# Optimization experiments

Hardware: AMD Instinct MI355X
Metric: run time of the kernel (lower is better)

## Reference

```python
import jax, jax.numpy as jnp
import numpy as np


def setup_inputs() -> dict:
    key = jax.random.key(0)
    ks = jax.random.split(key, 6)
    T, B, E = 2048, 4, 768
    x = jax.random.normal(ks[0], (T, B, E), dtype=jnp.float32)
    key_padding_mask = jax.random.randint(ks[1], (T, B), 0, 2).astype(jnp.bool_)
    attn_bias = jax.random.normal(ks[2], (T, B), dtype=jnp.float32)  # (src_len, bsz)
    in_proj_weight = jax.random.normal(ks[3], (3 * E, E), dtype=jnp.float32) * 0.02
    in_proj_bias = jnp.zeros((3 * E,), dtype=jnp.float32)
    out_weight = jax.random.normal(ks[4], (E, E), dtype=jnp.float32) * 0.02
    out_bias = jnp.zeros((E,), dtype=jnp.float32)
    return {
        "x": x,
        "key_padding_mask": key_padding_mask,
        "attn_bias": attn_bias,
        "in_proj_weight": in_proj_weight,
        "in_proj_bias": in_proj_bias,
        "out_weight": out_weight,
        "out_bias": out_bias,
        "num_heads": 12,
    }


def reference(x, key_padding_mask, attn_bias, in_proj_weight, in_proj_bias,
              out_weight, out_bias, num_heads):
    T, B, E = x.shape
    H = num_heads
    Dh = E // H
    scaling = Dh ** (-0.5)

    # fused QKV projection (self-attention path: q=k=v=x)
    qkv = x @ in_proj_weight.T + in_proj_bias        # (T, B, 3E)
    q, k, v = jnp.split(qkv, 3, axis=-1)             # each (T, B, E)
    q = q * scaling

    # (T, B, E) -> (B, H, T, Dh)
    def to_heads(t):
        return t.reshape(T, B, H, Dh).transpose(1, 2, 0, 3)
    q, k, v = to_heads(q), to_heads(k), to_heads(v)

    # scores: (B, H, T_tgt, T_src)
    scores = jnp.einsum('bhtd,bhsd->bhts', q, k)
    scores = scores + attn_bias.T[:, None, None, :]              # bias over src
    neg_inf = jnp.asarray(-jnp.inf, dtype=scores.dtype)
    scores = jnp.where(key_padding_mask.T[:, None, None, :], neg_inf, scores)

    weights = jax.nn.softmax(scores, axis=-1)
    attn = jnp.einsum('bhts,bhsd->bhtd', weights, v)             # (B, H, T, Dh)
    attn = attn.transpose(2, 0, 1, 3).reshape(T, B, E)           # (T, B, E)
    out = attn @ out_weight.T + out_bias
    return out
```

## Files before the change

### kernel.cpp

```cpp
#include <hip/hip_runtime.h>
#include <math.h>

#define T_LEN 2048
#define BSZ   4
#define EMB   768
#define NH    12
#define DH    64
#define NTOK  (T_LEN * BSZ)
#define N_QKV (3 * EMB)
#define BH    (BSZ * NH)
#define CONVB 8448

typedef _Float16 f16;
typedef _Float16 f16x8 __attribute__((ext_vector_type(8)));
typedef _Float16 f16x4 __attribute__((ext_vector_type(4)));
typedef float    f32x4 __attribute__((ext_vector_type(4)));

#define MFMA32(a, b, c) __builtin_amdgcn_mfma_f32_16x16x32_f16(a, b, c, 0, 0, 0)
#define MFMA16(a, b, c) __builtin_amdgcn_mfma_f32_16x16x16f16(a, b, c, 0, 0, 0)

__device__ __forceinline__ void gload16(const void* g, void* l) {
    __builtin_amdgcn_global_load_lds(
        (const __attribute__((address_space(1))) void*)g,
        (__attribute__((address_space(3))) void*)l, 16, 0, 0);
}

__global__ __launch_bounds__(256) void conv_compact(
    const float* __restrict__ s0, const float* __restrict__ s1,
    const float* __restrict__ s2, f16* __restrict__ dst,
    const int* __restrict__ mask, const float* __restrict__ abias,
    int* __restrict__ cidx, float* __restrict__ cbias,
    int* __restrict__ imap, int* __restrict__ ccount)
{
    const int tid = threadIdx.x;
    if (blockIdx.x < CONVB) {
        const int n0 = NTOK * EMB, n1 = N_QKV * EMB, n2 = EMB * EMB;
        const int i = (blockIdx.x * 256 + tid) * 4;
        const int t01 = n0 + n1;
        const float* s;
        int off;
        if (i < n0)            { s = s0; off = i; }
        else if (i < t01)      { s = s1; off = i - n0; }
        else if (i < t01 + n2) { s = s2; off = i - t01; }
        else return;
        const float4 v = *(const float4*)(s + off);
        f16 hv[4] = {(f16)v.x, (f16)v.y, (f16)v.z, (f16)v.w};
        *(double*)(dst + i) = *(double*)hv;
        return;
    }

    const int b = blockIdx.x - CONVB;
    __shared__ int cnt[32], off_l[32], tot[2];
    const int wv = tid >> 6, lane = tid & 63;
    int* ip = cidx + b * T_LEN;
    float* bp = cbias + b * T_LEN;
    int* mp = imap + b * T_LEN;

    for (int i = 0; i < 8; ++i) {
        const int c = wv * 8 + i;
        const int s = c * 64 + lane;
        const int mv = mask[s * BSZ + b];
        const unsigned long long bal = __ballot(mv == 0);
        if (lane == 0) cnt[c] = __popcll(bal);
    }
    __syncthreads();
    if (tid == 0) {
        int acc = 0;
        for (int c = 0; c < 32; ++c) { off_l[c] = acc; acc += cnt[c]; }
        const int npad = (acc + 63) & ~63;
        tot[0] = acc; tot[1] = npad;
        ccount[b] = npad;
    }
    __syncthreads();
    for (int i = 0; i < 8; ++i) {
        const int c = wv * 8 + i;
        const int s = c * 64 + lane;
        const int mv = mask[s * BSZ + b];
        const float bv = abias[s * BSZ + b];
        const unsigned long long bal = __ballot(mv == 0);
        const int pos = __popcll(bal & ((1ull << lane) - 1ull));
        const int basec = off_l[c];
        if (mv == 0) { ip[basec + pos] = s; bp[basec + pos] = bv; mp[s] = basec + pos; }
        else mp[s] = -1;
    }
    const int baseT = tot[0], npad = tot[1];
    if (tid < npad - baseT) { ip[baseT + tid] = 0; bp[baseT + tid] = -1e30f; }
}

template <int MODE>
__global__ __launch_bounds__(256) void gemm_h(
    const f16* __restrict__ A, const f16* __restrict__ W,
    const float* __restrict__ bias, float* __restrict__ C,
    f16* __restrict__ qb, f16* __restrict__ kc, f16* __restrict__ vb,
    const int* __restrict__ imap, int M, int N, int K)
{
    __shared__ __align__(16) f16 As[128][32];
    __shared__ __align__(16) f16 Bs[128][32];

    const int tid = threadIdx.x;
    const int w = tid >> 6, l = tid & 63;
    const int wr = w >> 1, wc = w & 1;
    const int lg = l >> 4, lr = l & 15;

    const int bm = blockIdx.x * 128, bn = blockIdx.y * 128;

    int srow[2], sqc[2];
#pragma unroll
    for (int it = 0; it < 2; ++it) {
        const int c = w * 128 + it * 64 + l;
        srow[it] = c >> 2;
        sqc[it] = (c & 3) ^ ((srow[it] >> 1) & 3);
    }

    f32x4 acc[4][4];
#pragma unroll
    for (int i = 0; i < 4; ++i)
#pragma unroll
        for (int j = 0; j < 4; ++j) acc[i][j] = (f32x4)(0.f);

    const int cq = lg ^ ((lr >> 1) & 3);

    for (int kt = 0; kt < K; kt += 32) {
        __syncthreads();
#pragma unroll
        for (int it = 0; it < 2; ++it) {
            const int ldsb = (w * 128 + it * 64) * 16;
            gload16(A + (size_t)(bm + srow[it]) * K + kt + sqc[it] * 8,
                    (char*)&As[0][0] + ldsb);
            gload16(W + (size_t)(bn + srow[it]) * K + kt + sqc[it] * 8,
                    (char*)&Bs[0][0] + ldsb);
        }
        __syncthreads();

        f16x8 af[4], bf[4];
#pragma unroll
        for (int am = 0; am < 4; ++am)
            af[am] = *(const f16x8*)((const char*)&As[0][0] +
                     (wr * 64 + am * 16 + lr) * 64 + cq * 16);
#pragma unroll
        for (int bnf = 0; bnf < 4; ++bnf)
            bf[bnf] = *(const f16x8*)((const char*)&Bs[0][0] +
                      (wc * 64 + bnf * 16 + lr) * 64 + cq * 16);
#pragma unroll
        for (int am = 0; am < 4; ++am)
#pragma unroll
            for (int bnf = 0; bnf < 4; ++bnf)
                acc[am][bnf] = MFMA32(af[am], bf[bnf], acc[am][bnf]);
    }

    const int colb = bn + wc * 64;
    const int rowb = bm + wr * 64;
    float bv[4];
#pragma unroll
    for (int j = 0; j < 4; ++j) bv[j] = bias[colb + j * 16 + lr];

    if (MODE == 0) {
#pragma unroll
        for (int am = 0; am < 4; ++am)
#pragma unroll
            for (int bnf = 0; bnf < 4; ++bnf)
#pragma unroll
                for (int rg = 0; rg < 4; ++rg) {
                    const int row = rowb + am * 16 + lg * 4 + rg;
                    const int col = colb + bnf * 16 + lr;
                    C[(size_t)row * N + col] = acc[am][bnf][rg] + bv[bnf];
                }
    } else {
        const int sec = bn / EMB;
        const float scale = (sec == 0) ? 0.125f : 1.0f;
#pragma unroll
        for (int bnf = 0; bnf < 4; ++bnf) {
            const int col = colb + bnf * 16 + lr;
            const int e = col - sec * EMB;
            const int h = e >> 6, d = e & 63;
#pragma unroll
            for (int am = 0; am < 4; ++am)
#pragma unroll
                for (int rg = 0; rg < 4; ++rg) {
                    const int row = rowb + am * 16 + lg * 4 + rg;
                    const int t = row >> 2, bb = row & 3;
                    const f16 val = (f16)((acc[am][bnf][rg] + bv[bnf]) * scale);
                    if (sec == 0) {
                        qb[((size_t)((bb * NH + h) * T_LEN + t)) * DH + d] = val;
                    } else if (sec == 1) {
                        const int ipv = imap[bb * T_LEN + t];
                        if (ipv >= 0)
                            kc[((size_t)((bb * NH + h) * T_LEN + ipv)) * DH + d] = val;
                    } else {
                        vb[((size_t)((bb * NH + h) * T_LEN + t)) * DH + d] = val;
                    }
                }
        }
    }
}

__global__ __launch_bounds__(256) void gather_vT(
    const f16* __restrict__ vb, const int* __restrict__ cidx,
    const int* __restrict__ ccnt, f16* __restrict__ vct)
{
    __shared__ f16 Vl[64][72];
    const int bh = blockIdx.y, b = bh / NH;
    const int i0 = blockIdx.x * 64;
    if (i0 >= ccnt[b]) return;
    const int tid = threadIdx.x;
    const size_t base = (size_t)bh * T_LEN * DH;

#pragma unroll
    for (int half = 0; half < 2; ++half) {
        const int c = half * 256 + tid;
        const int row = c >> 3, cc = c & 7;
        const int src = cidx[b * T_LEN + i0 + row];
        *(int4*)&Vl[row][cc * 8] =
            *(const int4*)(vb + base + (size_t)src * DH + cc * 8);
    }
    __syncthreads();
    const int dr = tid >> 2, ic = tid & 3;
    f16 tmp[16];
#pragma unroll
    for (int jj = 0; jj < 16; ++jj) tmp[jj] = Vl[ic * 16 + jj][dr];
    f16* dst = vct + ((size_t)bh * DH + dr) * T_LEN + i0 + ic * 16;
    *(int4*)(dst)     = *(int4*)&tmp[0];
    *(int4*)(dst + 8) = *(int4*)&tmp[8];
}

__global__ __launch_bounds__(256) void attn_mfma(
    const f16* __restrict__ qh, const f16* __restrict__ kcb,
    const f16* __restrict__ vct, const float* __restrict__ cbias,
    const int* __restrict__ ccnt, f16* __restrict__ abh)
{
    __shared__ __align__(16) f16 Kt[2][64][64];
    __shared__ __align__(16) f16 Vt[2][64][64];
    __shared__ float bias_l[2][64];

    const int bh = blockIdx.y, b = bh / NH, h = bh % NH;
    const int tid = threadIdx.x, w = tid >> 6, l = tid & 63;
    const int lg = l >> 4, lr = l & 15;
    const size_t base = (size_t)bh * T_LEN * DH;
    const int q0 = blockIdx.x * 128 + w * 32;

    f16x8 qf[2][2];
#pragma unroll
    for (int mi = 0; mi < 2; ++mi)
#pragma unroll
        for (int ki = 0; ki < 2; ++ki)
            qf[mi][ki] = *(const f16x8*)(qh + base +
                (size_t)(q0 + mi * 16 + lr) * DH + ki * 32 + lg * 8);

    f32x4 o[4][2];
#pragma unroll
    for (int dt = 0; dt < 4; ++dt)
#pragma unroll
        for (int mi = 0; mi < 2; ++mi) o[dt][mi] = (f32x4)(0.f);
    float m_[2] = {-1e30f, -1e30f}, l_[2] = {0.f, 0.f};

    const int npad = ccnt[b];
    const float* biasp = cbias + b * T_LEN;
    const f16* kbase = kcb + base;
    const f16* vtbase = vct + (size_t)bh * DH * T_LEN;

    int srow[2], scc[2];
#pragma unroll
    for (int it = 0; it < 2; ++it) {
        const int c = w * 128 + it * 64 + l;
        srow[it] = c >> 3;
        scc[it] = (c & 7) ^ (srow[it] & 7);
    }

    auto stage = [&](int buf, int i0s) {
#pragma unroll
        for (int it = 0; it < 2; ++it) {
            const int ldsb = (w * 128 + it * 64) * 16;
            gload16(kbase + (size_t)(i0s + srow[it]) * DH + scc[it] * 8,
                    (char*)&Kt[buf][0][0] + ldsb);
            gload16(vtbase + (size_t)srow[it] * T_LEN + i0s + scc[it] * 8,
                    (char*)&Vt[buf][0][0] + ldsb);
        }
        if (tid < 64) bias_l[buf][tid] = biasp[i0s + tid];
    };

    stage(0, 0);
    __syncthreads();

    int cur = 0;
    for (int i0 = 0; i0 < npad; i0 += 64, cur ^= 1) {
        if (i0 + 64 < npad) stage(cur ^ 1, i0 + 64);

        f32x4 s[4][2];
#pragma unroll
        for (int ni = 0; ni < 4; ++ni)
#pragma unroll
            for (int mi = 0; mi < 2; ++mi) s[ni][mi] = (f32x4)(0.f);
#pragma unroll
        for (int ni = 0; ni < 4; ++ni) {
            const int row = ni * 16 + lr;
#pragma unroll
            for (int ki = 0; ki < 2; ++ki) {
                const int cq = (ki * 4 + lg) ^ (row & 7);
                const f16x8 kf = *(const f16x8*)((const char*)&Kt[cur][0][0] +
                                 row * 128 + cq * 16);
#pragma unroll
                for (int mi = 0; mi < 2; ++mi)
                    s[ni][mi] = MFMA32(kf, qf[mi][ki], s[ni][mi]);
            }
        }

        float bv[4][4];
#pragma unroll
        for (int ni = 0; ni < 4; ++ni) {
            const float4 b4 = *(const float4*)&bias_l[cur][ni * 16 + lg * 4];
            bv[ni][0] = b4.x; bv[ni][1] = b4.y; bv[ni][2] = b4.z; bv[ni][3] = b4.w;
        }

        f16x4 pk[2][4];
        float r_[2];
#pragma unroll
        for (int mi = 0; mi < 2; ++mi) {
            float sv[4][4];
            float mx = -1e30f;
#pragma unroll
            for (int ni = 0; ni < 4; ++ni)
#pragma unroll
                for (int rg = 0; rg < 4; ++rg) {
                    sv[ni][rg] = s[ni][mi][rg] + bv[ni][rg];
                    mx = fmaxf(mx, sv[ni][rg]);
                }
            mx = fmaxf(mx, __shfl_xor(mx, 16));
            mx = fmaxf(mx, __shfl_xor(mx, 32));
            const float newm = fmaxf(m_[mi], mx);
            r_[mi] = __expf(m_[mi] - newm);
            m_[mi] = newm;
            float ps = 0.f;
#pragma unroll
            for (int ni = 0; ni < 4; ++ni) {
                float p0 = __expf(sv[ni][0] - newm);
                float p1 = __expf(sv[ni][1] - newm);
                float p2 = __expf(sv[ni][2] - newm);
                float p3 = __expf(sv[ni][3] - newm);
                ps += (p0 + p1) + (p2 + p3);
                pk[mi][ni] = (f16x4){(f16)p0, (f16)p1, (f16)p2, (f16)p3};
            }
            ps += __shfl_xor(ps, 16);
            ps += __shfl_xor(ps, 32);
            l_[mi] = l_[mi] * r_[mi] + ps;
        }

#pragma unroll
        for (int dt = 0; dt < 4; ++dt)
#pragma unroll
            for (int mi = 0; mi < 2; ++mi)
#pragma unroll
                for (int rg = 0; rg < 4; ++rg) o[dt][mi][rg] *= r_[mi];

#pragma unroll
        for (int dt = 0; dt < 4; ++dt) {
            const int row = dt * 16 + lr;
#pragma unroll
            for (int ni = 0; ni < 4; ++ni) {
                const int swc = (ni * 2 + (lg >> 1)) ^ (row & 7);
                const f16x4 vf = *(const f16x4*)((const char*)&Vt[cur][0][0] +
                                 row * 128 + swc * 16 + (lg & 1) * 8);
#pragma unroll
                for (int mi = 0; mi < 2; ++mi)
                    o[dt][mi] = MFMA16(vf, pk[mi][ni], o[dt][mi]);
            }
        }
        __syncthreads();
    }

#pragma unroll
    for (int mi = 0; mi < 2; ++mi) {
        const float inv = 1.f / l_[mi];
        const int q = q0 + mi * 16 + lr;
#pragma unroll
        for (int dt = 0; dt < 4; ++dt) {
            const int d0 = dt * 16 + lg * 4;
            f16x4 ov = {(f16)(o[dt][mi][0] * inv), (f16)(o[dt][mi][1] * inv),
                        (f16)(o[dt][mi][2] * inv), (f16)(o[dt][mi][3] * inv)};
            *(f16x4*)(abh + (size_t)(q * BSZ + b) * EMB + h * DH + d0) = ov;
        }
    }
}

extern "C" void kernel_launch(void* const* d_in, const int* in_sizes, int n_in,
                              void* d_out, int out_size, void* d_ws, size_t ws_size,
                              hipStream_t stream)
{
    const float* x     = (const float*)d_in[0];
    const int*   mask  = (const int*)d_in[1];
    const float* abias = (const float*)d_in[2];
    const float* wqkv  = (const float*)d_in[3];
    const float* bqkv  = (const float*)d_in[4];
    const float* wout  = (const float*)d_in[5];
    const float* bout  = (const float*)d_in[6];
    float* out = (float*)d_out;

    const int n_x  = NTOK * EMB;
    const int n_wq = N_QKV * EMB;
    const int n_wo = EMB * EMB;
    const size_t per = (size_t)BH * T_LEN * DH;

    f16* xh    = (f16*)d_ws;
    f16* wqkvh = xh + n_x;
    f16* wouth = wqkvh + n_wq;
    f16* qhb   = wouth + n_wo;
    f16* kcb   = qhb + per;
    f16* vhb   = kcb + per;
    f16* abh   = vhb + per;
    f16* vct   = abh + per;
    float* cbias = (float*)(vct + per);
    int*   cidx  = (int*)(cbias + BSZ * T_LEN);
    int*   imap  = cidx + BSZ * T_LEN;
    int*   ccnt  = imap + BSZ * T_LEN;

    conv_compact<<<CONVB + BSZ, 256, 0, stream>>>(
        x, wqkv, wout, xh, mask, abias, cidx, cbias, imap, ccnt);

    gemm_h<1><<<dim3(NTOK / 128, N_QKV / 128), 256, 0, stream>>>(
        xh, wqkvh, bqkv, nullptr, qhb, kcb, vhb, imap, NTOK, N_QKV, EMB);

    gather_vT<<<dim3(T_LEN / 64, BH), 256, 0, stream>>>(vhb, cidx, ccnt, vct);

    attn_mfma<<<dim3(T_LEN / 128, BH), 256, 0, stream>>>(
        qhb, kcb, vct, cbias, ccnt, abh);

    gemm_h<0><<<dim3(NTOK / 128, EMB / 128), 256, 0, stream>>>(
        abh, wouth, bout, out, nullptr, nullptr, nullptr, nullptr,
        NTOK, EMB, EMB);
}
```

Baseline: 246.1 us.

## Drop LDS staging in attention; read K/V fragments directly from global memory

```diff
diff --git a/kernel.cpp b/kernel.cpp
--- a/kernel.cpp
+++ b/kernel.cpp
@@ -223,15 +223,11 @@
     *(int4*)(dst + 8) = *(int4*)&tmp[8];
 }
 
-__global__ __launch_bounds__(256) void attn_mfma(
+__global__ __launch_bounds__(256, 3) void attn_mfma(
     const f16* __restrict__ qh, const f16* __restrict__ kcb,
     const f16* __restrict__ vct, const float* __restrict__ cbias,
     const int* __restrict__ ccnt, f16* __restrict__ abh)
 {
-    __shared__ __align__(16) f16 Kt[2][64][64];
-    __shared__ __align__(16) f16 Vt[2][64][64];
-    __shared__ float bias_l[2][64];
-
     const int bh = blockIdx.y, b = bh / NH, h = bh % NH;
     const int tid = threadIdx.x, w = tid >> 6, l = tid & 63;
     const int lg = l >> 4, lr = l & 15;
@@ -258,33 +254,7 @@
     const f16* kbase = kcb + base;
     const f16* vtbase = vct + (size_t)bh * DH * T_LEN;
 
-    int srow[2], scc[2];
-#pragma unroll
-    for (int it = 0; it < 2; ++it) {
-        const int c = w * 128 + it * 64 + l;
-        srow[it] = c >> 3;
-        scc[it] = (c & 7) ^ (srow[it] & 7);
-    }
-
-    auto stage = [&](int buf, int i0s) {
-#pragma unroll
-        for (int it = 0; it < 2; ++it) {
-            const int ldsb = (w * 128 + it * 64) * 16;
-            gload16(kbase + (size_t)(i0s + srow[it]) * DH + scc[it] * 8,
-                    (char*)&Kt[buf][0][0] + ldsb);
-            gload16(vtbase + (size_t)srow[it] * T_LEN + i0s + scc[it] * 8,
-                    (char*)&Vt[buf][0][0] + ldsb);
-        }
-        if (tid < 64) bias_l[buf][tid] = biasp[i0s + tid];
-    };
-
-    stage(0, 0);
-    __syncthreads();
-
-    int cur = 0;
-    for (int i0 = 0; i0 < npad; i0 += 64, cur ^= 1) {
-        if (i0 + 64 < npad) stage(cur ^ 1, i0 + 64);
-
+    for (int i0 = 0; i0 < npad; i0 += 64) {
         f32x4 s[4][2];
 #pragma unroll
         for (int ni = 0; ni < 4; ++ni)
@@ -292,12 +262,11 @@
             for (int mi = 0; mi < 2; ++mi) s[ni][mi] = (f32x4)(0.f);
 #pragma unroll
         for (int ni = 0; ni < 4; ++ni) {
-            const int row = ni * 16 + lr;
+            const int row = i0 + ni * 16 + lr;
 #pragma unroll
             for (int ki = 0; ki < 2; ++ki) {
-                const int cq = (ki * 4 + lg) ^ (row & 7);
-                const f16x8 kf = *(const f16x8*)((const char*)&Kt[cur][0][0] +
-                                 row * 128 + cq * 16);
+                const f16x8 kf = *(const f16x8*)(kbase +
+                    (size_t)row * DH + ki * 32 + lg * 8);
 #pragma unroll
                 for (int mi = 0; mi < 2; ++mi)
                     s[ni][mi] = MFMA32(kf, qf[mi][ki], s[ni][mi]);
@@ -307,7 +276,7 @@
         float bv[4][4];
 #pragma unroll
         for (int ni = 0; ni < 4; ++ni) {
-            const float4 b4 = *(const float4*)&bias_l[cur][ni * 16 + lg * 4];
+            const float4 b4 = *(const float4*)(biasp + i0 + ni * 16 + lg * 4);
             bv[ni][0] = b4.x; bv[ni][1] = b4.y; bv[ni][2] = b4.z; bv[ni][3] = b4.w;
         }
 
@@ -356,15 +325,13 @@
             const int row = dt * 16 + lr;
 #pragma unroll
             for (int ni = 0; ni < 4; ++ni) {
-                const int swc = (ni * 2 + (lg >> 1)) ^ (row & 7);
-                const f16x4 vf = *(const f16x4*)((const char*)&Vt[cur][0][0] +
-                                 row * 128 + swc * 16 + (lg & 1) * 8);
+                const f16x4 vf = *(const f16x4*)(vtbase +
+                    (size_t)row * T_LEN + i0 + ni * 16 + lg * 4);
 #pragma unroll
                 for (int mi = 0; mi < 2; ++mi)
                     o[dt][mi] = MFMA16(vf, pk[mi][ni], o[dt][mi]);
             }
         }
-        __syncthreads();
     }
 
 #pragma unroll
```

After: 349.0 us. 41.8% more time.

## Use 8 waves per attention block, exp2 softmax with lazy rescaling

Applied to the files above, without the earlier changes.

```diff
diff --git a/kernel.cpp b/kernel.cpp
--- a/kernel.cpp
+++ b/kernel.cpp
@@ -10,6 +10,7 @@
 #define N_QKV (3 * EMB)
 #define BH    (BSZ * NH)
 #define CONVB 8448
+#define LOG2E 1.44269504f
 
 typedef _Float16 f16;
 typedef _Float16 f16x8 __attribute__((ext_vector_type(8)));
@@ -80,8 +81,11 @@
         const unsigned long long bal = __ballot(mv == 0);
         const int pos = __popcll(bal & ((1ull << lane) - 1ull));
         const int basec = off_l[c];
-        if (mv == 0) { ip[basec + pos] = s; bp[basec + pos] = bv; mp[s] = basec + pos; }
-        else mp[s] = -1;
+        if (mv == 0) {
+            ip[basec + pos] = s;
+            bp[basec + pos] = bv * LOG2E;
+            mp[s] = basec + pos;
+        } else mp[s] = -1;
     }
     const int baseT = tot[0], npad = tot[1];
     if (tid < npad - baseT) { ip[baseT + tid] = 0; bp[baseT + tid] = -1e30f; }
@@ -167,7 +171,7 @@
                 }
     } else {
         const int sec = bn / EMB;
-        const float scale = (sec == 0) ? 0.125f : 1.0f;
+        const float scale = (sec == 0) ? (0.125f * LOG2E) : 1.0f;
 #pragma unroll
         for (int bnf = 0; bnf < 4; ++bnf) {
             const int col = colb + bnf * 16 + lr;
@@ -223,7 +227,7 @@
     *(int4*)(dst + 8) = *(int4*)&tmp[8];
 }
 
-__global__ __launch_bounds__(256) void attn_mfma(
+__global__ __launch_bounds__(512, 4) void attn_mfma(
     const f16* __restrict__ qh, const f16* __restrict__ kcb,
     const f16* __restrict__ vct, const float* __restrict__ cbias,
     const int* __restrict__ ccnt, f16* __restrict__ abh)
@@ -236,45 +240,33 @@
     const int tid = threadIdx.x, w = tid >> 6, l = tid & 63;
     const int lg = l >> 4, lr = l & 15;
     const size_t base = (size_t)bh * T_LEN * DH;
-    const int q0 = blockIdx.x * 128 + w * 32;
-
-    f16x8 qf[2][2];
-#pragma unroll
-    for (int mi = 0; mi < 2; ++mi)
-#pragma unroll
-        for (int ki = 0; ki < 2; ++ki)
-            qf[mi][ki] = *(const f16x8*)(qh + base +
-                (size_t)(q0 + mi * 16 + lr) * DH + ki * 32 + lg * 8);
-
-    f32x4 o[4][2];
-#pragma unroll
-    for (int dt = 0; dt < 4; ++dt)
-#pragma unroll
-        for (int mi = 0; mi < 2; ++mi) o[dt][mi] = (f32x4)(0.f);
-    float m_[2] = {-1e30f, -1e30f}, l_[2] = {0.f, 0.f};
+    const int q0 = blockIdx.x * 128 + w * 16;
+
+    f16x8 qf[2];
+#pragma unroll
+    for (int ki = 0; ki < 2; ++ki)
+        qf[ki] = *(const f16x8*)(qh + base +
+            (size_t)(q0 + lr) * DH + ki * 32 + lg * 8);
+
+    f32x4 o[4];
+#pragma unroll
+    for (int dt = 0; dt < 4; ++dt) o[dt] = (f32x4)(0.f);
+    float m_ = -1e30f, l_ = 0.f;
 
     const int npad = ccnt[b];
     const float* biasp = cbias + b * T_LEN;
     const f16* kbase = kcb + base;
     const f16* vtbase = vct + (size_t)bh * DH * T_LEN;
 
-    int srow[2], scc[2];
-#pragma unroll
-    for (int it = 0; it < 2; ++it) {
-        const int c = w * 128 + it * 64 + l;
-        srow[it] = c >> 3;
-        scc[it] = (c & 7) ^ (srow[it] & 7);
-    }
+    const int srow = tid >> 3;
+    const int scc  = (tid & 7) ^ (srow & 7);
+    const int ldsb = w * 1024;
 
     auto stage = [&](int buf, int i0s) {
-#pragma unroll
-        for (int it = 0; it < 2; ++it) {
-            const int ldsb = (w * 128 + it * 64) * 16;
-            gload16(kbase + (size_t)(i0s + srow[it]) * DH + scc[it] * 8,
-                    (char*)&Kt[buf][0][0] + ldsb);
-            gload16(vtbase + (size_t)srow[it] * T_LEN + i0s + scc[it] * 8,
-                    (char*)&Vt[buf][0][0] + ldsb);
-        }
+        gload16(kbase + (size_t)(i0s + srow) * DH + scc * 8,
+                (char*)&Kt[buf][0][0] + ldsb);
+        gload16(vtbase + (size_t)srow * T_LEN + i0s + scc * 8,
+                (char*)&Vt[buf][0][0] + ldsb);
         if (tid < 64) bias_l[buf][tid] = biasp[i0s + tid];
     };
 
@@ -285,11 +277,9 @@
     for (int i0 = 0; i0 < npad; i0 += 64, cur ^= 1) {
         if (i0 + 64 < npad) stage(cur ^ 1, i0 + 64);
 
-        f32x4 s[4][2];
-#pragma unroll
-        for (int ni = 0; ni < 4; ++ni)
-#pragma unroll
-            for (int mi = 0; mi < 2; ++mi) s[ni][mi] = (f32x4)(0.f);
+        f32x4 s[4];
+#pragma unroll
+        for (int ni = 0; ni < 4; ++ni) s[ni] = (f32x4)(0.f);
 #pragma unroll
         for (int ni = 0; ni < 4; ++ni) {
             const int row = ni * 16 + lr;
@@ -298,58 +288,50 @@
                 const int cq = (ki * 4 + lg) ^ (row & 7);
                 const f16x8 kf = *(const f16x8*)((const char*)&Kt[cur][0][0] +
                                  row * 128 + cq * 16);
-#pragma unroll
-                for (int mi = 0; mi < 2; ++mi)
-                    s[ni][mi] = MFMA32(kf, qf[mi][ki], s[ni][mi]);
+                s[ni] = MFMA32(kf, qf[ki], s[ni]);
             }
         }
 
-        float bv[4][4];
+        float sv[4][4];
+        float mx = -1e30f;
 #pragma unroll
         for (int ni = 0; ni < 4; ++ni) {
             const float4 b4 = *(const float4*)&bias_l[cur][ni * 16 + lg * 4];
-            bv[ni][0] = b4.x; bv[ni][1] = b4.y; bv[ni][2] = b4.z; bv[ni][3] = b4.w;
-        }
-
-        f16x4 pk[2][4];
-        float r_[2];
-#pragma unroll
-        for (int mi = 0; mi < 2; ++mi) {
-            float sv[4][4];
-            float mx = -1e30f;
-#pragma unroll
-            for (int ni = 0; ni < 4; ++ni)
-#pragma unroll
-                for (int rg = 0; rg < 4; ++rg) {
-                    sv[ni][rg] = s[ni][mi][rg] + bv[ni][rg];
-                    mx = fmaxf(mx, sv[ni][rg]);
-                }
-            mx = fmaxf(mx, __shfl_xor(mx, 16));
-            mx = fmaxf(mx, __shfl_xor(mx, 32));
-            const float newm = fmaxf(m_[mi], mx);
-            r_[mi] = __expf(m_[mi] - newm);
-            m_[mi] = newm;
-            float ps = 0.f;
-#pragma unroll
-            for (int ni = 0; ni < 4; ++ni) {
-                float p0 = __expf(sv[ni][0] - newm);
-                float p1 = __expf(sv[ni][1] - newm);
-                float p2 = __expf(sv[ni][2] - newm);
-                float p3 = __expf(sv[ni][3] - newm);
-                ps += (p0 + p1) + (p2 + p3);
-                pk[mi][ni] = (f16x4){(f16)p0, (f16)p1, (f16)p2, (f16)p3};
-            }
-            ps += __shfl_xor(ps, 16);
-            ps += __shfl_xor(ps, 32);
-            l_[mi] = l_[mi] * r_[mi] + ps;
-        }
-
-#pragma unroll
-        for (int dt = 0; dt < 4; ++dt)
-#pragma unroll
-            for (int mi = 0; mi < 2; ++mi)
-#pragma unroll
-                for (int rg = 0; rg < 4; ++rg) o[dt][mi][rg] *= r_[mi];
+            sv[ni][0] = s[ni][0] + b4.x;
+            sv[ni][1] = s[ni][1] + b4.y;
+            sv[ni][2] = s[ni][2] + b4.z;
+            sv[ni][3] = s[ni][3] + b4.w;
+            mx = fmaxf(mx, fmaxf(fmaxf(sv[ni][0], sv[ni][1]),
+                                 fmaxf(sv[ni][2], sv[ni][3])));
+        }
+        mx = fmaxf(mx, __shfl_xor(mx, 16));
+        mx = fmaxf(mx, __shfl_xor(mx, 32));
+
+        if (!__all(mx <= m_ + 11.0f)) {
+            const float newm = fmaxf(m_, mx);
+            const float r = exp2f(m_ - newm);
+            l_ *= r;
+#pragma unroll
+            for (int dt = 0; dt < 4; ++dt)
+#pragma unroll
+                for (int rg = 0; rg < 4; ++rg) o[dt][rg] *= r;
+            m_ = newm;
+        }
+
+        f16x4 pk[4];
+        float ps = 0.f;
+#pragma unroll
+        for (int ni = 0; ni < 4; ++ni) {
+            const float p0 = exp2f(sv[ni][0] - m_);
+            const float p1 = exp2f(sv[ni][1] - m_);
+            const float p2 = exp2f(sv[ni][2] - m_);
+            const float p3 = exp2f(sv[ni][3] - m_);
+            ps += (p0 + p1) + (p2 + p3);
+            pk[ni] = (f16x4){(f16)p0, (f16)p1, (f16)p2, (f16)p3};
+        }
+        ps += __shfl_xor(ps, 16);
+        ps += __shfl_xor(ps, 32);
+        l_ += ps;
 
 #pragma unroll
         for (int dt = 0; dt < 4; ++dt) {
@@ -359,25 +341,20 @@
                 const int swc = (ni * 2 + (lg >> 1)) ^ (row & 7);
                 const f16x4 vf = *(const f16x4*)((const char*)&Vt[cur][0][0] +
                                  row * 128 + swc * 16 + (lg & 1) * 8);
-#pragma unroll
-                for (int mi = 0; mi < 2; ++mi)
-                    o[dt][mi] = MFMA16(vf, pk[mi][ni], o[dt][mi]);
+                o[dt] = MFMA16(vf, pk[ni], o[dt]);
             }
         }
         __syncthreads();
     }
 
-#pragma unroll
-    for (int mi = 0; mi < 2; ++mi) {
-        const float inv = 1.f / l_[mi];
-        const int q = q0 + mi * 16 + lr;
-#pragma unroll
-        for (int dt = 0; dt < 4; ++dt) {
-            const int d0 = dt * 16 + lg * 4;
-            f16x4 ov = {(f16)(o[dt][mi][0] * inv), (f16)(o[dt][mi][1] * inv),
-                        (f16)(o[dt][mi][2] * inv), (f16)(o[dt][mi][3] * inv)};
-            *(f16x4*)(abh + (size_t)(q * BSZ + b) * EMB + h * DH + d0) = ov;
-        }
+    const float inv = 1.f / l_;
+    const int q = q0 + lr;
+#pragma unroll
+    for (int dt = 0; dt < 4; ++dt) {
+        const int d0 = dt * 16 + lg * 4;
+        f16x4 ov = {(f16)(o[dt][0] * inv), (f16)(o[dt][1] * inv),
+                    (f16)(o[dt][2] * inv), (f16)(o[dt][3] * inv)};
+        *(f16x4*)(abh + (size_t)(q * BSZ + b) * EMB + h * DH + d0) = ov;
     }
 }
 
@@ -420,7 +397,7 @@
 
     gather_vT<<<dim3(T_LEN / 64, BH), 256, 0, stream>>>(vhb, cidx, ccnt, vct);
 
-    attn_mfma<<<dim3(T_LEN / 128, BH), 256, 0, stream>>>(
+    attn_mfma<<<dim3(T_LEN / 128, BH), 512, 0, stream>>>(
         qhb, kcb, vct, cbias, ccnt, abh);
 
     gemm_h<0><<<dim3(NTOK / 128, EMB / 128), 256, 0, stream>>>(
```

After: 248.2 us. About the same (+0.8%).
